# Kernel optimization log

Hardware: AMD Instinct MI355X
Metric: run time of the kernel (lower is better)

Reference implementation:

```python
import jax, jax.numpy as jnp
import numpy as np

B, S, D, E2 = 64, 512, 1024, 1024  # batch, enc seq len, dec hidden, 2*enc hidden


def setup_inputs() -> dict:
    key = jax.random.key(0)
    ks = jax.random.split(key, 5)
    scale = 1.0 / np.sqrt(D + E2)
    return {
        "dec_state": jax.random.normal(ks[0], (B, D), jnp.float32),
        "enc_states": jax.random.normal(ks[1], (B, S, E2), jnp.float32),
        "att_mask": jnp.ones((B, S), jnp.int32),
        "w_weight": jax.random.normal(ks[2], (D, D + E2), jnp.float32) * scale,
        "w_bias": jax.random.normal(ks[3], (D,), jnp.float32) * scale,
        "v_weight": jax.random.normal(ks[4], (D,), jnp.float32) * (1.0 / np.sqrt(D)),
    }


def reference(dec_state, enc_states, att_mask, w_weight, w_bias, v_weight):
    # Additive (Bahdanau) attention. Split the concat-linear into two GEMMs:
    # tanh(W [dec; enc] + b) == tanh(dec @ Wd^T + enc @ We^T + b) -- same math,
    # avoids materializing the repeated/concatenated [B,S,D+2E] tensor.
    Wd = w_weight[:, :dec_state.shape[-1]]          # [D, D]
    We = w_weight[:, dec_state.shape[-1]:]          # [D, 2E]
    dec_proj = jnp.einsum('bd,kd->bk', dec_state, Wd)        # [B, D]
    enc_proj = jnp.einsum('bse,ke->bsk', enc_states, We)     # [B, S, D]
    energy = jnp.tanh(enc_proj + dec_proj[:, None, :] + w_bias)  # [B, S, D]
    attention = jnp.einsum('bsk,k->bs', energy, v_weight)    # [B, S]
    attention = jnp.where(att_mask == 0, -jnp.inf, attention)
    att_weights = jax.nn.softmax(attention, axis=1)          # [B, S]
    att_out = jnp.einsum('bs,bse->be', att_weights, enc_states)[:, None, :]  # [B,1,2E]
    return att_out
```

## Files before the change

### kernel.cpp

```cpp
#include <hip/hip_runtime.h>
#include <hip/hip_bf16.h>
#include <math.h>

#define B_  64
#define S_  512
#define D_  1024
#define E2_ 1024
#define WROW (D_ + E2_)
#define NTILES 4

typedef __attribute__((ext_vector_type(8))) short bf16x8;
typedef __attribute__((ext_vector_type(4))) float f32x4;
typedef __attribute__((ext_vector_type(8))) unsigned short u16x8;

__device__ __forceinline__ unsigned short f2bf(float f) {
    unsigned u = __float_as_uint(f);
    u = (u + 0x7FFFu + ((u >> 16) & 1u)) >> 16;
    return (unsigned short)u;
}

__device__ __forceinline__ float bf2f(unsigned short u) {
    return __uint_as_float((unsigned)u << 16);
}

__device__ __forceinline__ void load_lds16(const void* g, void* l) {
    __builtin_amdgcn_global_load_lds(
        (__attribute__((address_space(1))) void*)(void*)g,
        (__attribute__((address_space(3))) void*)l,
        16, 0, 0);
}

__device__ __forceinline__ float fast_tanh(float x) {
    float ax = fminf(fabsf(x), 16.0f);
    float t  = __builtin_amdgcn_exp2f(ax * 2.8853900817779268f);
    float r  = (t - 1.0f) * __builtin_amdgcn_rcpf(t + 1.0f);
    return copysignf(r, x);
}

__global__ __launch_bounds__(256) void conv_enc_kernel(
        const float* __restrict__ in, unsigned short* __restrict__ out, int n8)
{
    int i = blockIdx.x * 256 + threadIdx.x;
    const int stride = gridDim.x * 256;
    for (; i < n8; i += stride) {
        float4 a = *reinterpret_cast<const float4*>(in + (size_t)i * 8);
        float4 b = *reinterpret_cast<const float4*>(in + (size_t)i * 8 + 4);
        u16x8 o;
        o[0] = f2bf(a.x); o[1] = f2bf(a.y); o[2] = f2bf(a.z); o[3] = f2bf(a.w);
        o[4] = f2bf(b.x); o[5] = f2bf(b.y); o[6] = f2bf(b.z); o[7] = f2bf(b.w);
        *reinterpret_cast<u16x8*>(out + (size_t)i * 8) = o;
    }
}

__global__ __launch_bounds__(256) void conv_we_kernel(
        const float* __restrict__ w, unsigned short* __restrict__ web)
{
    const int k = blockIdx.x;
    const int j = threadIdx.x * 4;
    float4 a = *reinterpret_cast<const float4*>(w + (size_t)k * WROW + D_ + j);
    ushort4 o;
    o.x = f2bf(a.x); o.y = f2bf(a.y); o.z = f2bf(a.z); o.w = f2bf(a.w);
    *reinterpret_cast<ushort4*>(web + (size_t)k * E2_ + j) = o;
}

__global__ __launch_bounds__(256) void dec_proj_kernel(
        const float* __restrict__ dec,
        const float* __restrict__ w,
        const float* __restrict__ bias,
        float* __restrict__ t)
{
    __shared__ float wrow[D_];
    __shared__ float red[256];
    const int k = blockIdx.x;
    const int tid = threadIdx.x;

    const float* wr = w + (size_t)k * WROW;
    for (int i = tid; i < D_; i += 256) wrow[i] = wr[i];
    __syncthreads();

    const int b = tid >> 2;
    const int q = tid & 3;
    const float* dp = dec + b * D_ + q * 256;
    const float* wp = wrow + q * 256;
    float acc = 0.f;
    #pragma unroll 8
    for (int i = 0; i < 256; ++i) acc = fmaf(dp[i], wp[i], acc);
    red[tid] = acc;
    __syncthreads();
    if (q == 0) {
        float s = red[tid] + red[tid + 1] + red[tid + 2] + red[tid + 3];
        t[b * D_ + k] = s + bias[k];
    }
}

#define BME 256
#define BNE 256
#define BKE 64
#define KT_ (E2_ / BKE)

__global__ __launch_bounds__(512, 2) void energy_mfma_kernel(
        const unsigned short* __restrict__ encb,
        const unsigned short* __restrict__ web,
        const float* __restrict__ t,
        const float* __restrict__ v,
        float* __restrict__ att_part)
{
    __shared__ __align__(16) unsigned short As[2][BME * BKE];
    __shared__ __align__(16) unsigned short Bs[2][BNE * BKE];
    __shared__ float tv_s[BNE];
    __shared__ float vv_s[BNE];
    __shared__ float red[4][BME];

    const int g     = blockIdx.x;
    const int mblk  = (g & 7) + 8 * (g >> 5);
    const int ntile = (g >> 3) & 3;

    const int m0 = mblk * BME;
    const int n0 = ntile * BNE;
    const int b  = m0 >> 9;
    const int tid = threadIdx.x;
    const int w   = tid >> 6;
    const int l   = tid & 63;
    const int wm  = w >> 2;
    const int wn  = w & 3;

    if (tid < BNE) {
        tv_s[tid] = t[b * D_ + n0 + tid];
        vv_s[tid] = v[n0 + tid];
    }

    const int lr8 = l >> 3;
    const int lk  = 8 * ((l & 7) ^ lr8);
    const unsigned short* gA = encb + (size_t)m0 * E2_;
    const unsigned short* gB = web  + (size_t)n0 * E2_;

    const int rA = wm * 128 + (l & 15);
    const int rB = wn * 64 + (l & 15);
    const int kswz = (l & 7) << 4;
    const int khi  = (l >> 4) << 4;

    f32x4 acc[8][4] = {};

    auto stage = [&](int bf, int kt) {
        const int k0 = kt * BKE;
        #pragma unroll
        for (int r = 0; r < 4; ++r) {
            const int c = r * 8 + w;
            const int row = c * 8 + lr8;
            load_lds16(gA + (size_t)row * E2_ + k0 + lk,
                       (char*)As[bf] + c * 1024);
            load_lds16(gB + (size_t)row * E2_ + k0 + lk,
                       (char*)Bs[bf] + c * 1024);
        }
    };

    stage(0, 0);
    __syncthreads();

    for (int kt = 0; kt < KT_; ++kt) {
        const int cur = kt & 1;
        if (kt + 1 < KT_) stage(cur ^ 1, kt + 1);

        #pragma unroll
        for (int kk = 0; kk < 2; ++kk) {
            const int kb = (kk * 64 + khi) ^ kswz;
            bf16x8 a[8], bb[4];
            #pragma unroll
            for (int mi = 0; mi < 8; ++mi)
                a[mi] = *reinterpret_cast<const bf16x8*>(
                    (const char*)As[cur] + (rA + mi * 16) * 128 + kb);
            #pragma unroll
            for (int ni = 0; ni < 4; ++ni)
                bb[ni] = *reinterpret_cast<const bf16x8*>(
                    (const char*)Bs[cur] + (rB + ni * 16) * 128 + kb);
            __builtin_amdgcn_s_setprio(1);
            #pragma unroll
            for (int mi = 0; mi < 8; ++mi)
                #pragma unroll
                for (int ni = 0; ni < 4; ++ni)
                    acc[mi][ni] = __builtin_amdgcn_mfma_f32_16x16x32_bf16(
                        a[mi], bb[ni], acc[mi][ni], 0, 0, 0);
            __builtin_amdgcn_s_setprio(0);
        }
        __syncthreads();
    }

    #pragma unroll
    for (int mi = 0; mi < 8; ++mi) {
        float P[4] = {0.f, 0.f, 0.f, 0.f};
        #pragma unroll
        for (int ni = 0; ni < 4; ++ni) {
            const int nl = wn * 64 + ni * 16 + (l & 15);
            const float tvv = tv_s[nl];
            const float vvv = vv_s[nl];
            #pragma unroll
            for (int j = 0; j < 4; ++j) {
                float e = fast_tanh(acc[mi][ni][j] + tvv);
                P[j] = fmaf(e, vvv, P[j]);
            }
        }
        #pragma unroll
        for (int j = 0; j < 4; ++j) {
            float p = P[j];
            p += __shfl_xor(p, 1);
            p += __shfl_xor(p, 2);
            p += __shfl_xor(p, 4);
            p += __shfl_xor(p, 8);
            if ((l & 15) == 0)
                red[wn][wm * 128 + mi * 16 + (l >> 4) * 4 + j] = p;
        }
    }
    __syncthreads();
    if (tid < BME)
        att_part[(size_t)(m0 + tid) * NTILES + ntile] =
            (red[0][tid] + red[1][tid]) + (red[2][tid] + red[3][tid]);
}

__global__ __launch_bounds__(256) void softmax_kernel(
        const float* __restrict__ att_part,
        const int* __restrict__ mask,
        float* __restrict__ wout)
{
    __shared__ float red[256];
    const int b = blockIdx.x;
    const int tid = threadIdx.x;

    float x0 = 0.f, x1 = 0.f;
    #pragma unroll
    for (int p = 0; p < NTILES; ++p) {
        x0 += att_part[(size_t)(b * S_ + tid) * NTILES + p];
        x1 += att_part[(size_t)(b * S_ + 256 + tid) * NTILES + p];
    }
    bool m0v = (mask[b * S_ + tid] != 0);
    bool m1v = (mask[b * S_ + 256 + tid] != 0);
    if (!m0v) x0 = -INFINITY;
    if (!m1v) x1 = -INFINITY;

    float m = fmaxf(x0, x1);
    red[tid] = m;
    __syncthreads();
    for (int o = 128; o > 0; o >>= 1) {
        if (tid < o) red[tid] = fmaxf(red[tid], red[tid + o]);
        __syncthreads();
    }
    m = red[0];
    __syncthreads();

    float e0 = m0v ? expf(x0 - m) : 0.f;
    float e1 = m1v ? expf(x1 - m) : 0.f;
    red[tid] = e0 + e1;
    __syncthreads();
    for (int o = 128; o > 0; o >>= 1) {
        if (tid < o) red[tid] += red[tid + o];
        __syncthreads();
    }
    const float inv = 1.f / red[0];
    wout[b * S_ + tid] = e0 * inv;
    wout[b * S_ + 256 + tid] = e1 * inv;
}

__global__ __launch_bounds__(128) void attout_part_kernel(
        const float* __restrict__ wgt,
        const unsigned short* __restrict__ encb,
        float* __restrict__ out_part)
{
    __shared__ float wsm[64];
    const int b  = blockIdx.y;
    const int sc = blockIdx.x;
    const int tid = threadIdx.x;
    if (tid < 64) wsm[tid] = wgt[b * S_ + sc * 64 + tid];
    __syncthreads();

    const unsigned short* ep =
        encb + ((size_t)b * S_ + sc * 64) * E2_ + tid * 8;
    float acc[8] = {};
    #pragma unroll 4
    for (int s = 0; s < 64; ++s) {
        u16x8 e8 = *reinterpret_cast<const u16x8*>(ep + (size_t)s * E2_);
        const float ws = wsm[s];
        #pragma unroll
        for (int j = 0; j < 8; ++j)
            acc[j] = fmaf(ws, bf2f((unsigned short)e8[j]), acc[j]);
    }
    float* op = out_part + ((size_t)sc * B_ + b) * E2_ + tid * 8;
    #pragma unroll
    for (int j = 0; j < 8; ++j) op[j] = acc[j];
}

__global__ __launch_bounds__(256) void attout_reduce_kernel(
        const float* __restrict__ out_part,
        float* __restrict__ out)
{
    const int idx = blockIdx.x * 256 + threadIdx.x;
    const int n4 = (B_ * E2_) / 4;
    const float4* p = reinterpret_cast<const float4*>(out_part);
    float4 r = p[idx];
    #pragma unroll
    for (int c = 1; c < 8; ++c) {
        float4 q = p[idx + c * n4];
        r.x += q.x; r.y += q.y; r.z += q.z; r.w += q.w;
    }
    reinterpret_cast<float4*>(out)[idx] = r;
}

extern "C" void kernel_launch(void* const* d_in, const int* in_sizes, int n_in,
                              void* d_out, int out_size, void* d_ws, size_t ws_size,
                              hipStream_t stream) {
    const float* dec  = (const float*)d_in[0];
    const float* enc  = (const float*)d_in[1];
    const int*   mask = (const int*)d_in[2];
    const float* w    = (const float*)d_in[3];
    const float* bias = (const float*)d_in[4];
    const float* v    = (const float*)d_in[5];
    float* out = (float*)d_out;

    float* t_buf    = (float*)d_ws;
    float* att_part = t_buf + B_ * D_;
    float* wgt_buf  = att_part + B_ * S_ * NTILES;
    float* out_part = wgt_buf + B_ * S_;
    unsigned short* encb = (unsigned short*)(out_part + 8 * B_ * E2_);
    unsigned short* web  = encb + (size_t)B_ * S_ * E2_;

    const int enc_n8 = (B_ * S_ * E2_) / 8;
    conv_enc_kernel<<<4096, 256, 0, stream>>>(enc, encb, enc_n8);
    conv_we_kernel<<<D_, 256, 0, stream>>>(w, web);
    dec_proj_kernel<<<D_, 256, 0, stream>>>(dec, w, bias, t_buf);
    energy_mfma_kernel<<<512, 512, 0, stream>>>(encb, web, t_buf, v, att_part);
    softmax_kernel<<<B_, 256, 0, stream>>>(att_part, mask, wgt_buf);
    attout_part_kernel<<<dim3(8, B_), 128, 0, stream>>>(wgt_buf, encb, out_part);
    attout_reduce_kernel<<<(B_ * E2_ / 4) / 256, 256, 0, stream>>>(out_part, out);
}
```

Before: 161.1 us.

## Fuse fp32-to-bf16 conversion of encoder states into the energy GEMM loader

Removes the separate pass that converts the encoder states to bf16. The energy MFMA kernel now loads fp32 encoder tiles into registers, converts them, and writes swizzled bf16 into LDS, overlapping this with the MFMA work on the current buffer. The attention-output kernel reads fp32 encoder states directly with 256 threads. This drops one full read and write of the 128MB encoder tensor and a launch. The cost is that the energy GEMM now reads twice as many bytes for A, spends extra registers on the staged values, and does conversion work inside the main loop.

```diff
diff --git a/kernel.cpp b/kernel.cpp
--- a/kernel.cpp
+++ b/kernel.cpp
@@ -19,10 +19,6 @@
     return (unsigned short)u;
 }
 
-__device__ __forceinline__ float bf2f(unsigned short u) {
-    return __uint_as_float((unsigned)u << 16);
-}
-
 __device__ __forceinline__ void load_lds16(const void* g, void* l) {
     __builtin_amdgcn_global_load_lds(
         (__attribute__((address_space(1))) void*)(void*)g,
@@ -35,21 +31,6 @@
     float t  = __builtin_amdgcn_exp2f(ax * 2.8853900817779268f);
     float r  = (t - 1.0f) * __builtin_amdgcn_rcpf(t + 1.0f);
     return copysignf(r, x);
-}
-
-__global__ __launch_bounds__(256) void conv_enc_kernel(
-        const float* __restrict__ in, unsigned short* __restrict__ out, int n8)
-{
-    int i = blockIdx.x * 256 + threadIdx.x;
-    const int stride = gridDim.x * 256;
-    for (; i < n8; i += stride) {
-        float4 a = *reinterpret_cast<const float4*>(in + (size_t)i * 8);
-        float4 b = *reinterpret_cast<const float4*>(in + (size_t)i * 8 + 4);
-        u16x8 o;
-        o[0] = f2bf(a.x); o[1] = f2bf(a.y); o[2] = f2bf(a.z); o[3] = f2bf(a.w);
-        o[4] = f2bf(b.x); o[5] = f2bf(b.y); o[6] = f2bf(b.z); o[7] = f2bf(b.w);
-        *reinterpret_cast<u16x8*>(out + (size_t)i * 8) = o;
-    }
 }
 
 __global__ __launch_bounds__(256) void conv_we_kernel(
@@ -99,7 +80,7 @@
 #define KT_ (E2_ / BKE)
 
 __global__ __launch_bounds__(512, 2) void energy_mfma_kernel(
-        const unsigned short* __restrict__ encb,
+        const float* __restrict__ encf,
         const unsigned short* __restrict__ web,
         const float* __restrict__ t,
         const float* __restrict__ v,
@@ -129,10 +110,14 @@
         vv_s[tid] = v[n0 + tid];
     }
 
+    const int arow0 = tid >> 4;
+    const int acolb = (tid & 15) * 8;
+    const int aswz  = (arow0 & 7) << 4;
+    const float* gAf = encf + (size_t)m0 * E2_;
+
     const int lr8 = l >> 3;
     const int lk  = 8 * ((l & 7) ^ lr8);
-    const unsigned short* gA = encb + (size_t)m0 * E2_;
-    const unsigned short* gB = web  + (size_t)n0 * E2_;
+    const unsigned short* gB = web + (size_t)n0 * E2_;
 
     const int rA = wm * 128 + (l & 15);
     const int rB = wn * 64 + (l & 15);
@@ -141,25 +126,50 @@
 
     f32x4 acc[8][4] = {};
 
-    auto stage = [&](int bf, int kt) {
+    float4 av[8];
+    auto issueA = [&](int kt) {
+        const int k0 = kt * BKE;
+        #pragma unroll
+        for (int i = 0; i < 8; ++i) {
+            const int row = i * 32 + arow0;
+            av[i] = *reinterpret_cast<const float4*>(
+                gAf + (size_t)row * E2_ + k0 + (tid & 15) * 4);
+        }
+    };
+    auto issueB = [&](int bf, int kt) {
         const int k0 = kt * BKE;
         #pragma unroll
         for (int r = 0; r < 4; ++r) {
             const int c = r * 8 + w;
             const int row = c * 8 + lr8;
-            load_lds16(gA + (size_t)row * E2_ + k0 + lk,
-                       (char*)As[bf] + c * 1024);
             load_lds16(gB + (size_t)row * E2_ + k0 + lk,
                        (char*)Bs[bf] + c * 1024);
         }
     };
-
-    stage(0, 0);
+    auto writeA = [&](int bf) {
+        #pragma unroll
+        for (int i = 0; i < 8; ++i) {
+            const int row = i * 32 + arow0;
+            ushort4 o;
+            o.x = f2bf(av[i].x); o.y = f2bf(av[i].y);
+            o.z = f2bf(av[i].z); o.w = f2bf(av[i].w);
+            *reinterpret_cast<ushort4*>(
+                (char*)As[bf] + row * 128 + (acolb ^ aswz)) = o;
+        }
+    };
+
+    issueA(0);
+    issueB(0, 0);
+    writeA(0);
     __syncthreads();
 
     for (int kt = 0; kt < KT_; ++kt) {
         const int cur = kt & 1;
-        if (kt + 1 < KT_) stage(cur ^ 1, kt + 1);
+        const int nxt = cur ^ 1;
+        if (kt + 1 < KT_) {
+            issueA(kt + 1);
+            issueB(nxt, kt + 1);
+        }
 
         #pragma unroll
         for (int kk = 0; kk < 2; ++kk) {
@@ -182,6 +192,8 @@
                         a[mi], bb[ni], acc[mi][ni], 0, 0, 0);
             __builtin_amdgcn_s_setprio(0);
         }
+
+        if (kt + 1 < KT_) writeA(nxt);
         __syncthreads();
     }
 
@@ -259,9 +271,9 @@
     wout[b * S_ + 256 + tid] = e1 * inv;
 }
 
-__global__ __launch_bounds__(128) void attout_part_kernel(
+__global__ __launch_bounds__(256) void attout_part_kernel(
         const float* __restrict__ wgt,
-        const unsigned short* __restrict__ encb,
+        const float* __restrict__ enc,
         float* __restrict__ out_part)
 {
     __shared__ float wsm[64];
@@ -271,20 +283,19 @@
     if (tid < 64) wsm[tid] = wgt[b * S_ + sc * 64 + tid];
     __syncthreads();
 
-    const unsigned short* ep =
-        encb + ((size_t)b * S_ + sc * 64) * E2_ + tid * 8;
-    float acc[8] = {};
-    #pragma unroll 4
+    const float4* ep = reinterpret_cast<const float4*>(
+        enc + ((size_t)b * S_ + sc * 64) * E2_) + tid;
+    float4 acc = {0.f, 0.f, 0.f, 0.f};
+    #pragma unroll 8
     for (int s = 0; s < 64; ++s) {
-        u16x8 e8 = *reinterpret_cast<const u16x8*>(ep + (size_t)s * E2_);
+        float4 e4 = ep[(size_t)s * (E2_ / 4)];
         const float ws = wsm[s];
-        #pragma unroll
-        for (int j = 0; j < 8; ++j)
-            acc[j] = fmaf(ws, bf2f((unsigned short)e8[j]), acc[j]);
-    }
-    float* op = out_part + ((size_t)sc * B_ + b) * E2_ + tid * 8;
-    #pragma unroll
-    for (int j = 0; j < 8; ++j) op[j] = acc[j];
+        acc.x = fmaf(ws, e4.x, acc.x);
+        acc.y = fmaf(ws, e4.y, acc.y);
+        acc.z = fmaf(ws, e4.z, acc.z);
+        acc.w = fmaf(ws, e4.w, acc.w);
+    }
+    reinterpret_cast<float4*>(out_part + ((size_t)sc * B_ + b) * E2_)[tid] = acc;
 }
 
 __global__ __launch_bounds__(256) void attout_reduce_kernel(
@@ -318,15 +329,12 @@
     float* att_part = t_buf + B_ * D_;
     float* wgt_buf  = att_part + B_ * S_ * NTILES;
     float* out_part = wgt_buf + B_ * S_;
-    unsigned short* encb = (unsigned short*)(out_part + 8 * B_ * E2_);
-    unsigned short* web  = encb + (size_t)B_ * S_ * E2_;
-
-    const int enc_n8 = (B_ * S_ * E2_) / 8;
-    conv_enc_kernel<<<4096, 256, 0, stream>>>(enc, encb, enc_n8);
+    unsigned short* web = (unsigned short*)(out_part + 8 * B_ * E2_);
+
     conv_we_kernel<<<D_, 256, 0, stream>>>(w, web);
     dec_proj_kernel<<<D_, 256, 0, stream>>>(dec, w, bias, t_buf);
-    energy_mfma_kernel<<<512, 512, 0, stream>>>(encb, web, t_buf, v, att_part);
+    energy_mfma_kernel<<<512, 512, 0, stream>>>(enc, web, t_buf, v, att_part);
     softmax_kernel<<<B_, 256, 0, stream>>>(att_part, mask, wgt_buf);
-    attout_part_kernel<<<dim3(8, B_), 128, 0, stream>>>(wgt_buf, encb, out_part);
+    attout_part_kernel<<<dim3(8, B_), 256, 0, stream>>>(wgt_buf, enc, out_part);
     attout_reduce_kernel<<<(B_ * E2_ / 4) / 256, 256, 0, stream>>>(out_part, out);
 }
```

Measured after the change: 202.4 us. 25.6% more time.
